# Optimization experiments

Measured on AMD Instinct MI355X. Metric: run time of the kernel, lower is better.

Reference implementation:

```python
import jax, jax.numpy as jnp
import numpy as np
import math

HW = (14, 14)          # spatial token grid
L = HW[0] * HW[1]      # 196 spatial tokens
NUM_HEADS = 12
HEAD_DIM = 64
DIM = NUM_HEADS * HEAD_DIM
STEP_LEN = 4           # extension mode: 4 directions, step_length-1 = 3 entries
NUM_DIR = 4
NUM_ENTRY = STEP_LEN - 1
DE = NUM_DIR * NUM_ENTRY  # 12 table channels


def build_spatial_table() -> np.ndarray:
    """Dense [L, L, NUM_DIR*NUM_ENTRY] aggregation table (extension mode)."""
    Hh, Ww = HW
    table = np.zeros((L, L, DE), dtype=np.float32)
    for rank in range(L):
        h, w = divmod(rank, Ww)
        for step in range(1, STEP_LEN):
            dist = math.exp(-step ** 2 / STEP_LEN ** 2)
            se = step - 1
            top = rank - step * Ww
            bottom = rank + step * Ww
            left = rank - step
            right = rank + step
            if top >= 0:
                table[rank, top, 0 * NUM_ENTRY + se] = dist
            if bottom < L:
                table[rank, bottom, 1 * NUM_ENTRY + se] = dist
            if left >= 0 and left // Ww == h:
                table[rank, left, 2 * NUM_ENTRY + se] = dist
            if right < L and right // Ww == h:
                table[rank, right, 3 * NUM_ENTRY + se] = dist
    return table


def setup_inputs() -> dict:
    key = jax.random.key(0)
    ks = jax.random.split(key, 8)
    B, N = 64, L + 1  # +1 class token (skip=1)
    s_in = 1.0 / math.sqrt(DIM)
    inp = {
        "x": jax.random.normal(ks[0], (B, N, DIM), jnp.float32),
        "qkv_w": jax.random.normal(ks[1], (DIM, 3 * DIM), jnp.float32) * s_in,
        "qkv_b": jnp.zeros((3 * DIM,), jnp.float32),
        "proj_w": jax.random.normal(ks[2], (DIM, DIM), jnp.float32) * s_in,
        "proj_b": jnp.zeros((DIM,), jnp.float32),
        "wq": jax.random.normal(ks[3], (DE, NUM_HEADS), jnp.float32) * 0.02,
        "wk": jax.random.normal(ks[4], (DE, NUM_HEADS), jnp.float32) * 0.02,
        "wv": jax.random.normal(ks[5], (DE, NUM_HEADS), jnp.float32) * 0.02,
        "spatial_table": jnp.asarray(build_spatial_table()),
    }
    return inp


def _save_aggregate(v, table, w):
    """SAVE aggregation for one of q/k/v.

    v: [B, H, N, hd] with class token at position 0 (skipped).
    table: [L, L, DE] sparse positional aggregation weights.
    w: [DE, H] per-head channel mixing weights.
    Anchor buffer is identity -> residual add of the spatial tokens.
    """
    cls_tok, sp = v[:, :, :1, :], v[:, :, 1:, :]        # [B,H,1,hd], [B,H,L,hd]
    table_h = jnp.einsum('ije,eh->hij', table, w)       # [H, L, L]
    agg = sp + jnp.einsum('hij,bhjd->bhid', table_h, sp)
    return jnp.concatenate([cls_tok, agg], axis=2)


def reference(x, qkv_w, qkv_b, proj_w, proj_b, wq, wk, wv, spatial_table):
    B, N, C = x.shape
    H, hd = NUM_HEADS, HEAD_DIM
    scale = hd ** -0.5
    qkv = (x @ qkv_w + qkv_b).reshape(B, N, 3, H, hd)
    q, k, v = (jnp.transpose(qkv[:, :, i], (0, 2, 1, 3)) for i in range(3))  # [B,H,N,hd]
    q = _save_aggregate(q, spatial_table, wq)
    k = _save_aggregate(k, spatial_table, wk)
    v = _save_aggregate(v, spatial_table, wv)
    attn = jax.nn.softmax(jnp.einsum('bhid,bhjd->bhij', q, k) * scale, axis=-1)
    out = jnp.einsum('bhij,bhjd->bhid', attn, v)        # [B,H,N,hd]
    out = jnp.transpose(out, (0, 2, 1, 3)).reshape(B, N, C)
    return out @ proj_w + proj_b
```

## Files before the change

kernel.cpp:

```cpp
#include <hip/hip_runtime.h>

typedef unsigned short u16;
typedef __attribute__((ext_vector_type(8))) short short8;
typedef __attribute__((ext_vector_type(4))) float f32x4;

__device__ __forceinline__ u16 f2bf(float f) {
  unsigned u = __builtin_bit_cast(unsigned, f);
  u += 0x7FFFu + ((u >> 16) & 1u);
  return (u16)(u >> 16);
}
__device__ __forceinline__ float bf2f(u16 s) {
  unsigned u = ((unsigned)s) << 16;
  return __builtin_bit_cast(float, u);
}
__device__ __forceinline__ void gll16(const u16* g, u16* l) {
  __builtin_amdgcn_global_load_lds(
      (const __attribute__((address_space(1))) void*)g,
      (__attribute__((address_space(3))) void*)l, 16, 0, 0);
}

__global__ __launch_bounds__(256) void convert_f32_bf16(
    const float* __restrict__ in, u16* __restrict__ out, int n4) {
  int i = blockIdx.x * 256 + threadIdx.x;
  if (i >= n4) return;
  float4 v = ((const float4*)in)[i];
  ushort4 o;
  o.x = f2bf(v.x); o.y = f2bf(v.y); o.z = f2bf(v.z); o.w = f2bf(v.w);
  ((ushort4*)out)[i] = o;
}

__global__ __launch_bounds__(256) void transpose_f32_bf16(
    const float* __restrict__ in, u16* __restrict__ out, int R, int C) {
  __shared__ float tile[32][33];
  int c0 = blockIdx.x * 32, r0 = blockIdx.y * 32;
  int tx = threadIdx.x, ty = threadIdx.y;
  #pragma unroll
  for (int i = 0; i < 32; i += 8)
    tile[ty + i][tx] = in[(size_t)(r0 + ty + i) * C + c0 + tx];
  __syncthreads();
  #pragma unroll
  for (int i = 0; i < 32; i += 8)
    out[(size_t)(c0 + ty + i) * R + r0 + tx] = f2bf(tile[tx][ty + i]);
}

template<int MODE>
__global__ __launch_bounds__(256) void gemm_gll(
    const u16* __restrict__ A, const u16* __restrict__ Bt, int M, int NT,
    const float* __restrict__ bias, u16* __restrict__ ob, float* __restrict__ of) {
  constexpr int K = 768;
  __shared__ __align__(16) u16 Al[128 * 32];
  __shared__ __align__(16) u16 Bl[128 * 32];
  int tid = threadIdx.x, lane = tid & 63, w = tid >> 6;
  int nwg = gridDim.x, orig = blockIdx.x;
  int q = nwg >> 3, r = nwg & 7, xcd = orig & 7, slot = orig >> 3;
  int wg = (xcd < r ? xcd * (q + 1) : r * (q + 1) + (xcd - r) * q) + slot;
  int mt = wg / NT, nt = wg - mt * NT;
  int m0 = mt * 128, n0 = nt * 128;
  int wm = w >> 1, wn = w & 1;
  int lq = lane & 15, oct = lane >> 4;
  int srow = lane >> 2;
  int scol = (lane & 3) << 3;
  int ar0 = m0 + w * 16 + srow;      if (ar0 > M - 1) ar0 = M - 1;
  int ar1 = m0 + 64 + w * 16 + srow; if (ar1 > M - 1) ar1 = M - 1;
  const u16* ga0 = A + (size_t)ar0 * K + scol;
  const u16* ga1 = A + (size_t)ar1 * K + scol;
  const u16* gb0 = Bt + (size_t)(n0 + w * 16 + srow) * K + scol;
  const u16* gb1 = Bt + (size_t)(n0 + 64 + w * 16 + srow) * K + scol;
  u16* la0 = Al + w * 512;
  u16* la1 = Al + 2048 + w * 512;
  u16* lb0 = Bl + w * 512;
  u16* lb1 = Bl + 2048 + w * 512;
  f32x4 acc[4][4] = {};
  for (int kt = 0; kt < K; kt += 32) {
    gll16(ga0 + kt, la0);
    gll16(ga1 + kt, la1);
    gll16(gb0 + kt, lb0);
    gll16(gb1 + kt, lb1);
    __syncthreads();
    short8 af[4], bq[4];
    #pragma unroll
    for (int i = 0; i < 4; ++i)
      af[i] = *(const short8*)(Al + (wm * 64 + i * 16 + lq) * 32 + oct * 8);
    #pragma unroll
    for (int j = 0; j < 4; ++j)
      bq[j] = *(const short8*)(Bl + (wn * 64 + j * 16 + lq) * 32 + oct * 8);
    #pragma unroll
    for (int i = 0; i < 4; ++i)
      #pragma unroll
      for (int j = 0; j < 4; ++j)
        acc[i][j] = __builtin_amdgcn_mfma_f32_16x16x32_bf16(af[i], bq[j], acc[i][j], 0, 0, 0);
    __syncthreads();
  }
  int ldc = NT * 128;
  float bs[4];
  #pragma unroll
  for (int j = 0; j < 4; ++j) bs[j] = bias[n0 + wn * 64 + j * 16 + lq];
  #pragma unroll
  for (int i = 0; i < 4; ++i) {
    #pragma unroll
    for (int rr = 0; rr < 4; ++rr) {
      int m = m0 + wm * 64 + i * 16 + oct * 4 + rr;
      if (m < M) {
        #pragma unroll
        for (int j = 0; j < 4; ++j) {
          int c = n0 + wn * 64 + j * 16 + lq;
          float val = acc[i][j][rr] + bs[j];
          if (MODE == 0) ob[(size_t)m * ldc + c] = f2bf(val);
          else           of[(size_t)m * ldc + c] = val;
        }
      }
    }
  }
}

__global__ __launch_bounds__(256) void save_agg_fused(
    const u16* __restrict__ in, u16* __restrict__ q2, u16* __restrict__ k2,
    u16* __restrict__ v2, const float* __restrict__ wq,
    const float* __restrict__ wk, const float* __restrict__ wv) {
  constexpr int PER = 768 * 197 * 8;
  int vid = blockIdx.x * 256 + threadIdx.x;
  if (vid >= 3 * PER) return;
  int which = vid / PER;
  int rem = vid - which * PER;
  int dv = rem & 7;
  int n = (rem >> 3) % 197;
  int bh = rem / (197 * 8);
  int b = bh / 12, h = bh - b * 12;
  const float* w = (which == 0) ? wq : (which == 1) ? wk : wv;
  u16* outp = (which == 0) ? q2 : (which == 1) ? k2 : v2;
  size_t colbase = (size_t)which * 768 + h * 64 + dv * 8;
  const u16* rowp = in + (size_t)b * 197 * 2304 + colbase;
  size_t rowoff_out = ((size_t)bh * 197 + n) * 64 + dv * 8;
  uint4 cu = *(const uint4*)(rowp + (size_t)n * 2304);
  if (n == 0) { *(uint4*)(outp + rowoff_out) = cu; return; }
  union V8 { uint4 u; u16 s[8]; };
  V8 cv; cv.u = cu;
  float acc[8];
  #pragma unroll
  for (int j = 0; j < 8; ++j) acc[j] = bf2f(cv.s[j]);
  int rank = n - 1;
  int rw = rank % 14;
  const float dist[3] = {0.93941306281347579f, 0.77880078307140487f, 0.56978282473092302f};
  auto add = [&](int ntok, float wt) {
    V8 nv; nv.u = *(const uint4*)(rowp + (size_t)ntok * 2304);
    #pragma unroll
    for (int j = 0; j < 8; ++j) acc[j] += wt * bf2f(nv.s[j]);
  };
  #pragma unroll
  for (int s = 1; s <= 3; ++s) {
    float ds = dist[s - 1];
    if (rank - 14 * s >= 0)  add(n - 14 * s, ds * w[(0 + (s - 1)) * 12 + h]);
    if (rank + 14 * s < 196) add(n + 14 * s, ds * w[(3 + (s - 1)) * 12 + h]);
    if (rw - s >= 0)         add(n - s,      ds * w[(6 + (s - 1)) * 12 + h]);
    if (rw + s <= 13)        add(n + s,      ds * w[(9 + (s - 1)) * 12 + h]);
  }
  V8 ov;
  #pragma unroll
  for (int j = 0; j < 8; ++j) ov.s[j] = f2bf(acc[j]);
  *(uint4*)(outp + rowoff_out) = ov.u;
}

__global__ __launch_bounds__(256) void attn_kernel(
    const u16* __restrict__ q2, const u16* __restrict__ k2,
    const u16* __restrict__ v2, u16* __restrict__ attn_o) {
  __shared__ __align__(16) u16 Kl[208][72];
  __shared__ __align__(16) u16 Vt[64][232];
  __shared__ __align__(16) u16 Pl[4][16][40];
  int bh = blockIdx.x;
  int b = bh / 12, h = bh - b * 12;
  int tid = threadIdx.x, lane = tid & 63, wvid = tid >> 6;
  int lq = lane & 15, oct = lane >> 4;
  const u16* kb_ = k2 + (size_t)bh * 197 * 64;
  const u16* vb_ = v2 + (size_t)bh * 197 * 64;
  const u16* qb_ = q2 + (size_t)bh * 197 * 64;

  for (int idx = tid; idx < 208 * 8; idx += 256) {
    int r = idx >> 3, dv = idx & 7;
    uint4 val = make_uint4(0, 0, 0, 0);
    if (r < 197) val = *(const uint4*)(kb_ + (size_t)r * 64 + dv * 8);
    *(uint4*)(&Kl[r][dv * 8]) = val;
  }
  for (int idx = tid; idx < 224 * 8; idx += 256) {
    int r = idx >> 3, dv = idx & 7;
    union { uint4 u; u16 s[8]; } val;
    val.u = make_uint4(0, 0, 0, 0);
    if (r < 197) val.u = *(const uint4*)(vb_ + (size_t)r * 64 + dv * 8);
    #pragma unroll
    for (int j = 0; j < 8; ++j) Vt[dv * 8 + j][r] = val.s[j];
  }
  __syncthreads();

  for (int rt = wvid; rt < 13; rt += 4) {
    int qrow = rt * 16 + lq; if (qrow > 196) qrow = 196;
    short8 qa0 = *(const short8*)(qb_ + (size_t)qrow * 64 + oct * 8);
    short8 qa1 = *(const short8*)(qb_ + (size_t)qrow * 64 + 32 + oct * 8);
    f32x4 s[13];
    #pragma unroll
    for (int ct = 0; ct < 13; ++ct) {
      short8 k0 = *(const short8*)(&Kl[ct * 16 + lq][oct * 8]);
      short8 k1 = *(const short8*)(&Kl[ct * 16 + lq][32 + oct * 8]);
      f32x4 a = {0.f, 0.f, 0.f, 0.f};
      a = __builtin_amdgcn_mfma_f32_16x16x32_bf16(qa0, k0, a, 0, 0, 0);
      a = __builtin_amdgcn_mfma_f32_16x16x32_bf16(qa1, k1, a, 0, 0, 0);
      s[ct] = a;
    }
    float m[4] = {-3e38f, -3e38f, -3e38f, -3e38f};
    #pragma unroll
    for (int ct = 0; ct < 13; ++ct) {
      #pragma unroll
      for (int rr = 0; rr < 4; ++rr) {
        float v = s[ct][rr] * 0.125f;
        if (ct == 12 && lq >= 5) v = -1e30f;
        s[ct][rr] = v;
        m[rr] = fmaxf(m[rr], v);
      }
    }
    #pragma unroll
    for (int x = 1; x <= 8; x <<= 1) {
      #pragma unroll
      for (int rr = 0; rr < 4; ++rr) m[rr] = fmaxf(m[rr], __shfl_xor(m[rr], x, 64));
    }
    float rs[4] = {0.f, 0.f, 0.f, 0.f};
    #pragma unroll
    for (int ct = 0; ct < 13; ++ct) {
      #pragma unroll
      for (int rr = 0; rr < 4; ++rr) {
        float e = exp2f((s[ct][rr] - m[rr]) * 1.4426950408889634f);
        float er = bf2f(f2bf(e));
        s[ct][rr] = er;
        rs[rr] += er;
      }
    }
    #pragma unroll
    for (int x = 1; x <= 8; x <<= 1) {
      #pragma unroll
      for (int rr = 0; rr < 4; ++rr) rs[rr] += __shfl_xor(rs[rr], x, 64);
    }
    f32x4 oacc[4];
    #pragma unroll
    for (int dt = 0; dt < 4; ++dt) oacc[dt] = (f32x4){0.f, 0.f, 0.f, 0.f};
    #pragma unroll
    for (int ks = 0; ks < 7; ++ks) {
      #pragma unroll
      for (int tt = 0; tt < 2; ++tt) {
        int ct = ks * 2 + tt;
        #pragma unroll
        for (int rr = 0; rr < 4; ++rr) {
          u16 pu = 0;
          if (ct < 13) pu = f2bf(s[ct < 13 ? ct : 0][rr]);
          Pl[wvid][oct * 4 + rr][tt * 16 + lq] = pu;
        }
      }
      short8 pa = *(const short8*)(&Pl[wvid][lq][oct * 8]);
      #pragma unroll
      for (int dt = 0; dt < 4; ++dt) {
        short8 vbf = *(const short8*)(&Vt[dt * 16 + lq][ks * 32 + oct * 8]);
        oacc[dt] = __builtin_amdgcn_mfma_f32_16x16x32_bf16(pa, vbf, oacc[dt], 0, 0, 0);
      }
    }
    #pragma unroll
    for (int dt = 0; dt < 4; ++dt) {
      #pragma unroll
      for (int rr = 0; rr < 4; ++rr) {
        int qr = rt * 16 + oct * 4 + rr;
        if (qr < 197) {
          float val = oacc[dt][rr] / rs[rr];
          attn_o[(((size_t)b * 197 + qr) * 12 + h) * 64 + dt * 16 + lq] = f2bf(val);
        }
      }
    }
  }
}

extern "C" void kernel_launch(void* const* d_in, const int* in_sizes, int n_in,
                              void* d_out, int out_size, void* d_ws, size_t ws_size,
                              hipStream_t stream) {
  const float* x      = (const float*)d_in[0];
  const float* qkv_w  = (const float*)d_in[1];
  const float* qkv_b  = (const float*)d_in[2];
  const float* proj_w = (const float*)d_in[3];
  const float* proj_b = (const float*)d_in[4];
  const float* wq     = (const float*)d_in[5];
  const float* wk     = (const float*)d_in[6];
  const float* wv     = (const float*)d_in[7];
  float* out = (float*)d_out;

  constexpr size_t SZ = 9682944;
  u16* ws = (u16*)d_ws;
  u16* xb   = ws;
  u16* wT   = xb + SZ;
  u16* pT   = wT + 2304 * 768;
  u16* qkvb = pT + 768 * 768;
  u16* q2   = qkvb + 3 * SZ;
  u16* k2   = q2 + SZ;
  u16* v2   = k2 + SZ;
  u16* ao   = xb;

  convert_f32_bf16<<<dim3(9456), dim3(256), 0, stream>>>(x, xb, 2420736);
  transpose_f32_bf16<<<dim3(72, 24), dim3(32, 8), 0, stream>>>(qkv_w, wT, 768, 2304);
  transpose_f32_bf16<<<dim3(24, 24), dim3(32, 8), 0, stream>>>(proj_w, pT, 768, 768);
  gemm_gll<0><<<dim3(99 * 18), dim3(256), 0, stream>>>(xb, wT, 12608, 18, qkv_b, qkvb, nullptr);
  save_agg_fused<<<dim3(14184), dim3(256), 0, stream>>>(qkvb, q2, k2, v2, wq, wk, wv);
  attn_kernel<<<dim3(768), dim3(256), 0, stream>>>(q2, k2, v2, ao);
  gemm_gll<1><<<dim3(99 * 6), dim3(256), 0, stream>>>(ao, pT, 12608, 6, proj_b, nullptr, out);
}
```

Measured before the change: 298.1 us.

## Fuse SAVE aggregation into attention kernel, reading QKV directly

```diff
diff --git a/kernel.cpp b/kernel.cpp
--- a/kernel.cpp
+++ b/kernel.cpp
@@ -113,56 +113,51 @@
   }
 }
 
-__global__ __launch_bounds__(256) void save_agg_fused(
-    const u16* __restrict__ in, u16* __restrict__ q2, u16* __restrict__ k2,
-    u16* __restrict__ v2, const float* __restrict__ wq,
-    const float* __restrict__ wk, const float* __restrict__ wv) {
-  constexpr int PER = 768 * 197 * 8;
-  int vid = blockIdx.x * 256 + threadIdx.x;
-  if (vid >= 3 * PER) return;
-  int which = vid / PER;
-  int rem = vid - which * PER;
-  int dv = rem & 7;
-  int n = (rem >> 3) % 197;
-  int bh = rem / (197 * 8);
-  int b = bh / 12, h = bh - b * 12;
-  const float* w = (which == 0) ? wq : (which == 1) ? wk : wv;
-  u16* outp = (which == 0) ? q2 : (which == 1) ? k2 : v2;
-  size_t colbase = (size_t)which * 768 + h * 64 + dv * 8;
-  const u16* rowp = in + (size_t)b * 197 * 2304 + colbase;
-  size_t rowoff_out = ((size_t)bh * 197 + n) * 64 + dv * 8;
-  uint4 cu = *(const uint4*)(rowp + (size_t)n * 2304);
-  if (n == 0) { *(uint4*)(outp + rowoff_out) = cu; return; }
-  union V8 { uint4 u; u16 s[8]; };
-  V8 cv; cv.u = cu;
+__device__ __forceinline__ void agg_row16(
+    const u16* __restrict__ p, int n, const float cw[4][3], u16 out[8]) {
+  union V8 { uint4 u; u16 s[8]; } c;
+  c.u = *(const uint4*)p;
+  if (n == 0) {
+    #pragma unroll
+    for (int j = 0; j < 8; ++j) out[j] = c.s[j];
+    return;
+  }
   float acc[8];
   #pragma unroll
-  for (int j = 0; j < 8; ++j) acc[j] = bf2f(cv.s[j]);
+  for (int j = 0; j < 8; ++j) acc[j] = bf2f(c.s[j]);
   int rank = n - 1;
   int rw = rank % 14;
-  const float dist[3] = {0.93941306281347579f, 0.77880078307140487f, 0.56978282473092302f};
-  auto add = [&](int ntok, float wt) {
-    V8 nv; nv.u = *(const uint4*)(rowp + (size_t)ntok * 2304);
-    #pragma unroll
-    for (int j = 0; j < 8; ++j) acc[j] += wt * bf2f(nv.s[j]);
-  };
-  #pragma unroll
-  for (int s = 1; s <= 3; ++s) {
-    float ds = dist[s - 1];
-    if (rank - 14 * s >= 0)  add(n - 14 * s, ds * w[(0 + (s - 1)) * 12 + h]);
-    if (rank + 14 * s < 196) add(n + 14 * s, ds * w[(3 + (s - 1)) * 12 + h]);
-    if (rw - s >= 0)         add(n - s,      ds * w[(6 + (s - 1)) * 12 + h]);
-    if (rw + s <= 13)        add(n + s,      ds * w[(9 + (s - 1)) * 12 + h]);
-  }
-  V8 ov;
-  #pragma unroll
-  for (int j = 0; j < 8; ++j) ov.s[j] = f2bf(acc[j]);
-  *(uint4*)(outp + rowoff_out) = ov.u;
-}
-
-__global__ __launch_bounds__(256) void attn_kernel(
-    const u16* __restrict__ q2, const u16* __restrict__ k2,
-    const u16* __restrict__ v2, u16* __restrict__ attn_o) {
+  #pragma unroll
+  for (int s_ = 1; s_ <= 3; ++s_) {
+    if (rank - 14 * s_ >= 0) {
+      V8 nv; nv.u = *(const uint4*)(p - 14 * s_ * 2304);
+      #pragma unroll
+      for (int j = 0; j < 8; ++j) acc[j] += cw[0][s_ - 1] * bf2f(nv.s[j]);
+    }
+    if (rank + 14 * s_ < 196) {
+      V8 nv; nv.u = *(const uint4*)(p + 14 * s_ * 2304);
+      #pragma unroll
+      for (int j = 0; j < 8; ++j) acc[j] += cw[1][s_ - 1] * bf2f(nv.s[j]);
+    }
+    if (rw - s_ >= 0) {
+      V8 nv; nv.u = *(const uint4*)(p - s_ * 2304);
+      #pragma unroll
+      for (int j = 0; j < 8; ++j) acc[j] += cw[2][s_ - 1] * bf2f(nv.s[j]);
+    }
+    if (rw + s_ <= 13) {
+      V8 nv; nv.u = *(const uint4*)(p + s_ * 2304);
+      #pragma unroll
+      for (int j = 0; j < 8; ++j) acc[j] += cw[3][s_ - 1] * bf2f(nv.s[j]);
+    }
+  }
+  #pragma unroll
+  for (int j = 0; j < 8; ++j) out[j] = f2bf(acc[j]);
+}
+
+__global__ __launch_bounds__(256) void attn_agg_kernel(
+    const u16* __restrict__ qkv, const float* __restrict__ wq,
+    const float* __restrict__ wk, const float* __restrict__ wv,
+    u16* __restrict__ attn_o) {
   __shared__ __align__(16) u16 Kl[208][72];
   __shared__ __align__(16) u16 Vt[64][232];
   __shared__ __align__(16) u16 Pl[4][16][40];
@@ -170,38 +165,51 @@
   int b = bh / 12, h = bh - b * 12;
   int tid = threadIdx.x, lane = tid & 63, wvid = tid >> 6;
   int lq = lane & 15, oct = lane >> 4;
-  const u16* kb_ = k2 + (size_t)bh * 197 * 64;
-  const u16* vb_ = v2 + (size_t)bh * 197 * 64;
-  const u16* qb_ = q2 + (size_t)bh * 197 * 64;
+  const u16* base = qkv + (size_t)b * 197 * 2304 + h * 64;
+
+  const float dist[3] = {0.93941306281347579f, 0.77880078307140487f, 0.56978282473092302f};
+  float cwq[4][3], cwk[4][3], cwv[4][3];
+  #pragma unroll
+  for (int d_ = 0; d_ < 4; ++d_)
+    #pragma unroll
+    for (int s_ = 0; s_ < 3; ++s_) {
+      int e = (d_ * 3 + s_) * 12 + h;
+      cwq[d_][s_] = dist[s_] * wq[e];
+      cwk[d_][s_] = dist[s_] * wk[e];
+      cwv[d_][s_] = dist[s_] * wv[e];
+    }
 
   for (int idx = tid; idx < 208 * 8; idx += 256) {
     int r = idx >> 3, dv = idx & 7;
-    uint4 val = make_uint4(0, 0, 0, 0);
-    if (r < 197) val = *(const uint4*)(kb_ + (size_t)r * 64 + dv * 8);
-    *(uint4*)(&Kl[r][dv * 8]) = val;
+    union { uint4 u; u16 s[8]; } o;
+    o.u = make_uint4(0, 0, 0, 0);
+    if (r < 197) agg_row16(base + 768 + (size_t)r * 2304 + dv * 8, r, cwk, o.s);
+    *(uint4*)(&Kl[r][dv * 8]) = o.u;
   }
   for (int idx = tid; idx < 224 * 8; idx += 256) {
     int r = idx >> 3, dv = idx & 7;
-    union { uint4 u; u16 s[8]; } val;
-    val.u = make_uint4(0, 0, 0, 0);
-    if (r < 197) val.u = *(const uint4*)(vb_ + (size_t)r * 64 + dv * 8);
-    #pragma unroll
-    for (int j = 0; j < 8; ++j) Vt[dv * 8 + j][r] = val.s[j];
+    union { uint4 u; u16 s[8]; } o;
+    o.u = make_uint4(0, 0, 0, 0);
+    if (r < 197) agg_row16(base + 1536 + (size_t)r * 2304 + dv * 8, r, cwv, o.s);
+    #pragma unroll
+    for (int j = 0; j < 8; ++j) Vt[dv * 8 + j][r] = o.s[j];
   }
   __syncthreads();
 
   for (int rt = wvid; rt < 13; rt += 4) {
     int qrow = rt * 16 + lq; if (qrow > 196) qrow = 196;
-    short8 qa0 = *(const short8*)(qb_ + (size_t)qrow * 64 + oct * 8);
-    short8 qa1 = *(const short8*)(qb_ + (size_t)qrow * 64 + 32 + oct * 8);
+    const u16* qp = base + (size_t)qrow * 2304;
+    union { short8 v; u16 s[8]; } qa0, qa1;
+    agg_row16(qp + oct * 8, qrow, cwq, qa0.s);
+    agg_row16(qp + 32 + oct * 8, qrow, cwq, qa1.s);
     f32x4 s[13];
     #pragma unroll
     for (int ct = 0; ct < 13; ++ct) {
       short8 k0 = *(const short8*)(&Kl[ct * 16 + lq][oct * 8]);
       short8 k1 = *(const short8*)(&Kl[ct * 16 + lq][32 + oct * 8]);
       f32x4 a = {0.f, 0.f, 0.f, 0.f};
-      a = __builtin_amdgcn_mfma_f32_16x16x32_bf16(qa0, k0, a, 0, 0, 0);
-      a = __builtin_amdgcn_mfma_f32_16x16x32_bf16(qa1, k1, a, 0, 0, 0);
+      a = __builtin_amdgcn_mfma_f32_16x16x32_bf16(qa0.v, k0, a, 0, 0, 0);
+      a = __builtin_amdgcn_mfma_f32_16x16x32_bf16(qa1.v, k1, a, 0, 0, 0);
       s[ct] = a;
     }
     float m[4] = {-3e38f, -3e38f, -3e38f, -3e38f};
@@ -291,16 +299,12 @@
   u16* wT   = xb + SZ;
   u16* pT   = wT + 2304 * 768;
   u16* qkvb = pT + 768 * 768;
-  u16* q2   = qkvb + 3 * SZ;
-  u16* k2   = q2 + SZ;
-  u16* v2   = k2 + SZ;
   u16* ao   = xb;
 
   convert_f32_bf16<<<dim3(9456), dim3(256), 0, stream>>>(x, xb, 2420736);
   transpose_f32_bf16<<<dim3(72, 24), dim3(32, 8), 0, stream>>>(qkv_w, wT, 768, 2304);
   transpose_f32_bf16<<<dim3(24, 24), dim3(32, 8), 0, stream>>>(proj_w, pT, 768, 768);
   gemm_gll<0><<<dim3(99 * 18), dim3(256), 0, stream>>>(xb, wT, 12608, 18, qkv_b, qkvb, nullptr);
-  save_agg_fused<<<dim3(14184), dim3(256), 0, stream>>>(qkvb, q2, k2, v2, wq, wk, wv);
-  attn_kernel<<<dim3(768), dim3(256), 0, stream>>>(q2, k2, v2, ao);
+  attn_agg_kernel<<<dim3(768), dim3(256), 0, stream>>>(qkvb, wq, wk, wv, ao);
   gemm_gll<1><<<dim3(99 * 6), dim3(256), 0, stream>>>(ao, pT, 12608, 6, proj_b, nullptr, out);
 }
```

Result: slower. 341.2 us (+14.5%).
